# Kernel optimization log

Hardware: AMD Instinct MI355X
Metric: run time of the kernel (lower is better)

Reference implementation:

```python
import jax, jax.numpy as jnp
import numpy as np

N = 100000   # nodes
E = 1600000  # edges (avg degree 16)
D = 64       # feature / hidden / embedding dim
OUT = 2
NEG_SLOPE = 0.2


def setup_inputs() -> dict:
    key = jax.random.key(0)
    ks = jax.random.split(key, 12)
    s = 1.0 / np.sqrt(D)
    return {
        "x": jax.random.normal(ks[0], (N, D), dtype=jnp.float32),
        "edge_index": jax.random.randint(ks[1], (2, E), 0, N, dtype=jnp.int64),
        "Wl": jax.random.normal(ks[2], (3, D, D), dtype=jnp.float32) * s,
        "bl": jnp.zeros((3, D), dtype=jnp.float32),
        "Wr": jax.random.normal(ks[3], (3, D, D), dtype=jnp.float32) * s,
        "br": jnp.zeros((3, D), dtype=jnp.float32),
        "att": jax.random.normal(ks[4], (3, D), dtype=jnp.float32) * s,
        "bg": jnp.zeros((3, D), dtype=jnp.float32),
        "Ws": jax.random.normal(ks[5], (3, D, D), dtype=jnp.float32) * s,
        "bs": jnp.zeros((3, D), dtype=jnp.float32),
        "Wout": jax.random.normal(ks[6], (D, OUT), dtype=jnp.float32) * s,
        "bout": jnp.zeros((OUT,), dtype=jnp.float32),
    }


def _gatv2(h, src, dst, Wl, bl, Wr, br, att, bg):
    # GATv2Conv (heads=1, concat, add_self_loops=False):
    #   e_ij = att . LeakyReLU(Wl h_j + Wr h_i); softmax over incoming edges of i;
    #   out_i = sum_j alpha_ij * (Wl h_j) + bias
    xl = h @ Wl + bl                      # [N, D] source transform
    xr = h @ Wr + br                      # [N, D] dest transform
    e = jax.nn.leaky_relu(xl[src] + xr[dst], NEG_SLOPE) @ att  # [E]
    m = jax.ops.segment_max(e, dst, num_segments=N)            # per-dest max
    a = jnp.exp(e - m[dst])                                    # [E]
    denom = jax.ops.segment_sum(a, dst, num_segments=N)        # [N]
    alpha = a / denom[dst]                                     # [E]
    agg = jax.ops.segment_sum(alpha[:, None] * xl[src], dst, num_segments=N)
    return agg + bg                                            # [N, D]


def reference(x, edge_index, Wl, bl, Wr, br, att, bg, Ws, bs, Wout, bout):
    src, dst = edge_index[0], edge_index[1]
    # layer 1: gat1 + skip1, relu (dropout_rate=0 -> identity)
    h = jax.nn.relu(_gatv2(x, src, dst, Wl[0], bl[0], Wr[0], br[0], att[0], bg[0])
                    + x @ Ws[0] + bs[0])
    # middle layer
    h = jax.nn.relu(_gatv2(h, src, dst, Wl[1], bl[1], Wr[1], br[1], att[1], bg[1])
                    + h @ Ws[1] + bs[1])
    # last gat layer: no relu after
    h = _gatv2(h, src, dst, Wl[2], bl[2], Wr[2], br[2], att[2], bg[2]) + h @ Ws[2] + bs[2]
    return h @ Wout + bout
```

## Files before the change

kernel.cpp:

```cpp
#include <hip/hip_runtime.h>
#include <stdint.h>

#define NN 100000
#define EE 1600000
#define DD 64
#define NBUCK 782
#define SCWG 800
#define SCCHUNK 2000

using short8 = __attribute__((ext_vector_type(8))) short;
using f32x4  = __attribute__((ext_vector_type(4))) float;
using f2     = __attribute__((ext_vector_type(2))) float;


__device__ __forceinline__ unsigned short bf16_rne(float f) {
    unsigned int u = __float_as_uint(f);
    unsigned int r = (u + 0x7FFFu + ((u >> 16) & 1u)) >> 16;
    return (unsigned short)r;
}
__device__ __forceinline__ float bf16_to_f32(unsigned short h) {
    return __uint_as_float(((unsigned int)h) << 16);
}


__global__ void bucket_hist(const int* __restrict__ dst, int* __restrict__ bhist) {
    __shared__ int h[NBUCK];
    int t = threadIdx.x;
    for (int b = t; b < NBUCK; b += 256) h[b] = 0;
    __syncthreads();
    int start = blockIdx.x * SCCHUNK;
    int endi = min(start + SCCHUNK, EE);
    for (int e = start + t; e < endi; e += 256)
        atomicAdd(&h[dst[e] >> 7], 1);
    __syncthreads();
    for (int b = t; b < NBUCK; b += 256)
        if (h[b]) atomicAdd(&bhist[b], h[b]);
}

__global__ void bucket_scan(const int* __restrict__ bhist, int* __restrict__ bbase,
                            int* __restrict__ bcursor, int* __restrict__ offsets) {
    __shared__ int s[1024];
    int t = threadIdx.x;
    int v = (t < NBUCK) ? bhist[t] : 0;
    s[t] = v;
    __syncthreads();
    for (int off = 1; off < 1024; off <<= 1) {
        int a = (t >= off) ? s[t - off] : 0;
        __syncthreads();
        s[t] += a;
        __syncthreads();
    }
    if (t < NBUCK) { int excl = s[t] - v; bbase[t] = excl; bcursor[t] = excl; }
    if (t == 0) { bbase[NBUCK] = EE; offsets[NN] = EE; }
}

__global__ void bucket_scatter(const int* __restrict__ src, const int* __restrict__ dst,
                               int* __restrict__ bcursor, unsigned int* __restrict__ bedges) {
    __shared__ int cnt[NBUCK];
    __shared__ int lcur[NBUCK];
    int t = threadIdx.x;
    for (int b = t; b < NBUCK; b += 256) cnt[b] = 0;
    __syncthreads();
    int start = blockIdx.x * SCCHUNK;
    int endi = min(start + SCCHUNK, EE);
    for (int e = start + t; e < endi; e += 256)
        atomicAdd(&cnt[dst[e] >> 7], 1);
    __syncthreads();
    for (int b = t; b < NBUCK; b += 256) {
        int c = cnt[b];
        lcur[b] = c ? atomicAdd(&bcursor[b], c) : 0;
    }
    __syncthreads();
    for (int e = start + t; e < endi; e += 256) {
        int d = dst[e];
        int pos = atomicAdd(&lcur[d >> 7], 1);
        bedges[pos] = ((unsigned int)(d & 127) << 24) | (unsigned int)src[e];
    }
}

__global__ void bucket_csr(const unsigned int* __restrict__ bedges, const int* __restrict__ bbase,
                           int* __restrict__ offsets, int* __restrict__ csr) {
    __shared__ int ncnt[128];
    __shared__ int lofs[128];
    int b = blockIdx.x;
    int t = threadIdx.x;
    int beg = bbase[b], endb = bbase[b + 1];
    if (t < 128) ncnt[t] = 0;
    __syncthreads();
    for (int e = beg + t; e < endb; e += 256)
        atomicAdd(&ncnt[bedges[e] >> 24], 1);
    __syncthreads();
    if (t < 128) lofs[t] = ncnt[t];
    __syncthreads();
    for (int off = 1; off < 128; off <<= 1) {
        int a = 0;
        if (t < 128 && t >= off) a = lofs[t - off];
        __syncthreads();
        if (t < 128) lofs[t] += a;
        __syncthreads();
    }
    int excl = 0;
    if (t < 128) {
        excl = lofs[t] - ncnt[t];
        int node = b * 128 + t;
        if (node < NN) offsets[node] = beg + excl;
    }
    __syncthreads();
    if (t < 128) ncnt[t] = beg + excl;
    __syncthreads();
    for (int e = beg + t; e < endb; e += 256) {
        unsigned int ed = bedges[e];
        int pos = atomicAdd(&ncnt[ed >> 24], 1);
        csr[pos] = (int)(ed & 0xFFFFFFu);
    }
}


__global__ void conv_wx(const float* __restrict__ Wl, const float* __restrict__ Wr,
                        const float* __restrict__ Ws, const float* __restrict__ x,
                        unsigned short* __restrict__ Wt_hi, unsigned short* __restrict__ Wt_lo,
                        unsigned short* __restrict__ Ahi) {
    if (blockIdx.x < 144) {
        int e = blockIdx.x * 256 + threadIdx.x;
        if (e >= 9 * 4096) return;
        int mat = e >> 12;
        int r   = e & 4095;
        int k   = r >> 6, n = r & 63;
        int L = mat / 3, j = mat % 3;
        const float* W = (j == 0) ? Wl : ((j == 1) ? Wr : Ws);
        float v = W[L * 4096 + k * 64 + n];
        unsigned short hi = bf16_rne(v);
        unsigned short lo = bf16_rne(v - bf16_to_f32(hi));
        Wt_hi[mat * 4096 + n * 64 + k] = hi;
        Wt_lo[mat * 4096 + n * 64 + k] = lo;
    } else {
        int i = (blockIdx.x - 144) * 256 + threadIdx.x;
        int total = NN * 16;
        int stride = (gridDim.x - 144) * 256;
        for (; i < total; i += stride) {
            float4 v = *(const float4*)&x[(size_t)i * 4];
            ushort4 h;
            h.x = bf16_rne(v.x);
            h.y = bf16_rne(v.y);
            h.z = bf16_rne(v.z);
            h.w = bf16_rne(v.w);
            *(ushort4*)&Ahi[(size_t)i * 4] = h;
        }
    }
}


__global__ __launch_bounds__(256) void gemm_mfma(
    const unsigned short* __restrict__ Ahi,
    const unsigned short* __restrict__ Wt_hi, const unsigned short* __restrict__ Wt_lo,
    const float* __restrict__ bl, const float* __restrict__ br, const float* __restrict__ bs,
    unsigned short* __restrict__ Xlb, unsigned short* __restrict__ XRS) {
    int lane = threadIdx.x & 63;
    int wid  = threadIdx.x >> 6;
    int m0 = (blockIdx.x * 4 + wid) * 32;
    if (m0 >= NN) return;

    int l4 = lane & 15;
    int hi = lane >> 4;
    int koff = hi * 8;

    int arow0 = m0 + l4, arow1 = m0 + 16 + l4;
    bool ok0 = arow0 < NN, ok1 = arow1 < NN;
    int ar0 = ok0 ? arow0 : NN - 1;
    int ar1 = ok1 ? arow1 : NN - 1;

    const unsigned short* ab0 = Ahi + (size_t)ar0 * 64;
    const unsigned short* ab1 = Ahi + (size_t)ar1 * 64;
    short8 a0k0 = *(const short8*)(ab0 + koff);
    short8 a0k1 = *(const short8*)(ab0 + 32 + koff);
    short8 a1k0 = *(const short8*)(ab1 + koff);
    short8 a1k1 = *(const short8*)(ab1 + 32 + koff);

    int nbase0 = hi * 4;

#pragma unroll
    for (int m = 0; m < 3; m++) {
        const unsigned short* wh = Wt_hi + m * 4096;
        const unsigned short* wl = Wt_lo + m * 4096;
        const float* bias = (m == 0) ? bl : ((m == 1) ? br : bs);
#pragma unroll
        for (int tt = 0; tt < 4; tt++) {
            int ncol = tt * 16 + l4;
            const unsigned short* bh = wh + ncol * 64 + koff;
            const unsigned short* blo = wl + ncol * 64 + koff;
            short8 bhi0 = *(const short8*)bh;
            short8 bhi1 = *(const short8*)(bh + 32);
            short8 blo0 = *(const short8*)blo;
            short8 blo1 = *(const short8*)(blo + 32);

            f32x4 acc0 = {0.f, 0.f, 0.f, 0.f};
            f32x4 acc1 = {0.f, 0.f, 0.f, 0.f};
            acc0 = __builtin_amdgcn_mfma_f32_16x16x32_bf16(bhi0, a0k0, acc0, 0, 0, 0);
            acc1 = __builtin_amdgcn_mfma_f32_16x16x32_bf16(bhi0, a1k0, acc1, 0, 0, 0);
            acc0 = __builtin_amdgcn_mfma_f32_16x16x32_bf16(bhi1, a0k1, acc0, 0, 0, 0);
            acc1 = __builtin_amdgcn_mfma_f32_16x16x32_bf16(bhi1, a1k1, acc1, 0, 0, 0);
            acc0 = __builtin_amdgcn_mfma_f32_16x16x32_bf16(blo0, a0k0, acc0, 0, 0, 0);
            acc1 = __builtin_amdgcn_mfma_f32_16x16x32_bf16(blo0, a1k0, acc1, 0, 0, 0);
            acc0 = __builtin_amdgcn_mfma_f32_16x16x32_bf16(blo1, a0k1, acc0, 0, 0, 0);
            acc1 = __builtin_amdgcn_mfma_f32_16x16x32_bf16(blo1, a1k1, acc1, 0, 0, 0);

            int nb = tt * 16 + nbase0;
            float4 bb = *(const float4*)&bias[nb];
            ushort4 h0, h1;
            h0.x = bf16_rne(acc0[0] + bb.x); h0.y = bf16_rne(acc0[1] + bb.y);
            h0.z = bf16_rne(acc0[2] + bb.z); h0.w = bf16_rne(acc0[3] + bb.w);
            h1.x = bf16_rne(acc1[0] + bb.x); h1.y = bf16_rne(acc1[1] + bb.y);
            h1.z = bf16_rne(acc1[2] + bb.z); h1.w = bf16_rne(acc1[3] + bb.w);
            if (m == 0) {
                if (ok0) *(ushort4*)&Xlb[(size_t)ar0 * 64 + nb] = h0;
                if (ok1) *(ushort4*)&Xlb[(size_t)ar1 * 64 + nb] = h1;
            } else {
                int coff = (m == 1) ? 0 : 64;
                if (ok0) *(ushort4*)&XRS[(size_t)ar0 * 128 + coff + nb] = h0;
                if (ok1) *(ushort4*)&XRS[(size_t)ar1 * 128 + coff + nb] = h1;
            }
        }
    }
}


__device__ __forceinline__ float group_sum16(float t) {
    t += __int_as_float(__builtin_amdgcn_update_dpp(0, __float_as_int(t), 0xB1, 0xF, 0xF, true));
    t += __int_as_float(__builtin_amdgcn_update_dpp(0, __float_as_int(t), 0x4E, 0xF, 0xF, true));
    t += __int_as_float(__builtin_amdgcn_update_dpp(0, __float_as_int(t), 0x141, 0xF, 0xF, true));
    t += __int_as_float(__builtin_amdgcn_update_dpp(0, __float_as_int(t), 0x140, 0xF, 0xF, true));
    return t;
}

__device__ __forceinline__ void unpack4(uint2 u, f2& v01, f2& v23) {
    v01 = f2{ __uint_as_float(u.x << 16), __uint_as_float(u.x & 0xFFFF0000u) };
    v23 = f2{ __uint_as_float(u.y << 16), __uint_as_float(u.y & 0xFFFF0000u) };
}

__global__ __launch_bounds__(256) void node_kernel(
    const unsigned short* __restrict__ Xlb, const unsigned short* __restrict__ XRS,
    const int* __restrict__ offsets, const int* __restrict__ csr,
    const float* __restrict__ att, const float* __restrict__ bg,
    unsigned short* __restrict__ hout, int do_relu,
    const float* __restrict__ Wout, const float* __restrict__ bout,
    float* __restrict__ outp, int do_out) {
    int lane = threadIdx.x & 63;
    int wid  = threadIdx.x >> 6;
    int i = blockIdx.x * 4 + wid;
    if (i >= NN) return;
    int sub = lane & 15;
    int grp = lane >> 4;

    f2 xr01, xr23;
    unpack4(*(const uint2*)&XRS[(size_t)i * 128 + sub * 4], xr01, xr23);
    float4 att4 = *(const float4*)&att[sub * 4];
    f2 at01 = {att4.x, att4.y}, at23 = {att4.z, att4.w};

    f2 agg01 = {0.f, 0.f}, agg23 = {0.f, 0.f};
    float denom = 0.f;
    int beg = offsets[i], end = offsets[i + 1];

    for (int j0 = beg; j0 < end; j0 += 8) {
        int jA = j0 + grp, jB = jA + 4;
        bool vA = jA < end, vB = jB < end;
        int sA = csr[vA ? jA : beg];
        int sB = csr[vB ? jB : beg];
        uint2 uA = *(const uint2*)&Xlb[(size_t)sA * 64 + sub * 4];
        uint2 uB = *(const uint2*)&Xlb[(size_t)sB * 64 + sub * 4];
        f2 xA01, xA23, xB01, xB23;
        unpack4(uA, xA01, xA23);
        unpack4(uB, xB01, xB23);

        f2 sA01 = xA01 + xr01;
        f2 sA23 = xA23 + xr23;
        f2 sB01 = xB01 + xr01;
        f2 sB23 = xB23 + xr23;
        f2 lA01 = { fmaxf(sA01.x, 0.2f * sA01.x), fmaxf(sA01.y, 0.2f * sA01.y) };
        f2 lA23 = { fmaxf(sA23.x, 0.2f * sA23.x), fmaxf(sA23.y, 0.2f * sA23.y) };
        f2 lB01 = { fmaxf(sB01.x, 0.2f * sB01.x), fmaxf(sB01.y, 0.2f * sB01.y) };
        f2 lB23 = { fmaxf(sB23.x, 0.2f * sB23.x), fmaxf(sB23.y, 0.2f * sB23.y) };

        f2 tAv = lA01 * at01 + lA23 * at23;
        f2 tBv = lB01 * at01 + lB23 * at23;
        float tA = group_sum16(tAv.x + tAv.y);
        float tB = group_sum16(tBv.x + tBv.y);
        float aA = vA ? __expf(tA) : 0.f;
        float aB = vB ? __expf(tB) : 0.f;

        f2 aAv = {aA, aA};
        f2 aBv = {aB, aB};
        agg01 += aAv * xA01 + aBv * xB01;
        agg23 += aAv * xA23 + aBv * xB23;
        denom += aA + aB;
    }

    float aggx = agg01.x, aggy = agg01.y, aggz = agg23.x, aggw = agg23.y;
#pragma unroll
    for (int m = 16; m <= 32; m <<= 1) {
        aggx  += __shfl_xor(aggx, m, 64);
        aggy  += __shfl_xor(aggy, m, 64);
        aggz  += __shfl_xor(aggz, m, 64);
        aggw  += __shfl_xor(aggw, m, 64);
        denom += __shfl_xor(denom, m, 64);
    }

    float inv = (denom > 0.f) ? (1.0f / denom) : 0.f;
    f2 sk01, sk23;
    unpack4(*(const uint2*)&XRS[(size_t)i * 128 + 64 + sub * 4], sk01, sk23);
    float4 bg4 = *(const float4*)&bg[sub * 4];
    float4 res;
    res.x = aggx * inv + bg4.x + sk01.x;
    res.y = aggy * inv + bg4.y + sk01.y;
    res.z = aggz * inv + bg4.z + sk23.x;
    res.w = aggw * inv + bg4.w + sk23.y;
    if (do_relu) {
        res.x = fmaxf(res.x, 0.f); res.y = fmaxf(res.y, 0.f);
        res.z = fmaxf(res.z, 0.f); res.w = fmaxf(res.w, 0.f);
    }
    if (do_out) {
        float4 w01 = *(const float4*)&Wout[8 * sub];
        float4 w23 = *(const float4*)&Wout[8 * sub + 4];
        float o0 = res.x * w01.x + res.y * w01.z + res.z * w23.x + res.w * w23.z;
        float o1 = res.x * w01.y + res.y * w01.w + res.z * w23.y + res.w * w23.w;
        o0 = group_sum16(o0);
        o1 = group_sum16(o1);
        if (lane == 0) {
            outp[(size_t)i * 2 + 0] = o0 + bout[0];
            outp[(size_t)i * 2 + 1] = o1 + bout[1];
        }
    } else {
        if (grp == 0) {
            ushort4 h;
            h.x = bf16_rne(res.x);
            h.y = bf16_rne(res.y);
            h.z = bf16_rne(res.z);
            h.w = bf16_rne(res.w);
            *(ushort4*)&hout[(size_t)i * 64 + sub * 4] = h;
        }
    }
}


extern "C" void kernel_launch(void* const* d_in, const int* in_sizes, int n_in,
                              void* d_out, int out_size, void* d_ws, size_t ws_size,
                              hipStream_t stream) {
    const float* x    = (const float*)d_in[0];
    const int*   ei   = (const int*)d_in[1];
    const float* Wl   = (const float*)d_in[2];
    const float* bl   = (const float*)d_in[3];
    const float* Wr   = (const float*)d_in[4];
    const float* br   = (const float*)d_in[5];
    const float* att  = (const float*)d_in[6];
    const float* bg   = (const float*)d_in[7];
    const float* Ws   = (const float*)d_in[8];
    const float* bs   = (const float*)d_in[9];
    const float* Wout = (const float*)d_in[10];
    const float* bout = (const float*)d_in[11];
    float* out = (float*)d_out;

    size_t off = 0;
    char* base = (char*)d_ws;
    auto alloc = [&](size_t bytes) -> void* {
        void* p = base + off;
        off += (bytes + 255) & ~(size_t)255;
        return p;
    };
    unsigned short* Xlb = (unsigned short*)alloc((size_t)NN * 64 * 2);
    unsigned short* XRS = (unsigned short*)alloc((size_t)NN * 128 * 2);
    unsigned short* Ahi = (unsigned short*)alloc((size_t)NN * 64 * 2);
    unsigned short* Bhi = (unsigned short*)alloc((size_t)NN * 64 * 2);
    unsigned short* Wthi = (unsigned short*)alloc((size_t)9 * 4096 * 2);
    unsigned short* Wtlo = (unsigned short*)alloc((size_t)9 * 4096 * 2);
    int*  bhist  = (int*)alloc((size_t)NBUCK * 4);
    int*  bbase  = (int*)alloc((size_t)(NBUCK + 1) * 4);
    int*  bcur   = (int*)alloc((size_t)NBUCK * 4);
    unsigned int* bedges = (unsigned int*)alloc((size_t)EE * 4);
    int*  offs   = (int*)alloc((size_t)(NN + 1) * 4);
    int*  csr    = (int*)alloc((size_t)EE * 4);

    const int* src = ei;
    const int* dst = ei + EE;

    hipMemsetAsync(bhist, 0, (size_t)NBUCK * 4, stream);
    bucket_hist<<<SCWG, 256, 0, stream>>>(dst, bhist);
    bucket_scan<<<1, 1024, 0, stream>>>(bhist, bbase, bcur, offs);
    bucket_scatter<<<SCWG, 256, 0, stream>>>(src, dst, bcur, bedges);
    bucket_csr<<<NBUCK, 256, 0, stream>>>(bedges, bbase, offs, csr);

    conv_wx<<<144 + 400, 256, 0, stream>>>(Wl, Wr, Ws, x, Wthi, Wtlo, Ahi);

    unsigned short* cur = Ahi;
    unsigned short* nxt = Bhi;
    for (int L = 0; L < 3; L++) {
        gemm_mfma<<<(NN + 127) / 128, 256, 0, stream>>>(
            cur, Wthi + (size_t)L * 3 * 4096, Wtlo + (size_t)L * 3 * 4096,
            bl + L * 64, br + L * 64, bs + L * 64, Xlb, XRS);
        node_kernel<<<NN / 4, 256, 0, stream>>>(
            Xlb, XRS, offs, csr, att + L * 64, bg + L * 64,
            nxt, (L < 2) ? 1 : 0,
            Wout, bout, out, (L == 2) ? 1 : 0);
        unsigned short* tp = cur; cur = nxt; nxt = tp;
    }
}
```

Before: 356.4 us.

## Fuse CSR build and weight/input conversion into one cooperative kernel

Replaces the memset and five separate preprocessing launches (histogram, scan, scatter, per-bucket CSR, weight/x bf16 conversion) with a single cooperative kernel that separates the phases with grid-wide syncs. If the cooperative launch fails, it falls back to five phase-indexed launches. The aim is to remove per-launch overhead and idle gaps between the small preprocessing kernels. In exchange it adds grid-barrier cost, and 800 blocks must be co-resident for the cooperative launch to succeed.

Result: slower. 728.4 us (+104.4%).

```diff
diff --git a/kernel.cpp b/kernel.cpp
--- a/kernel.cpp
+++ b/kernel.cpp
@@ -1,5 +1,8 @@
 #include <hip/hip_runtime.h>
+#include <hip/hip_cooperative_groups.h>
 #include <stdint.h>
+
+namespace cg = cooperative_groups;
 
 #define NN 100000
 #define EE 1600000
@@ -23,128 +26,135 @@
 }
 
 
-__global__ void bucket_hist(const int* __restrict__ dst, int* __restrict__ bhist) {
-    __shared__ int h[NBUCK];
+__global__ __launch_bounds__(256) void csr_conv_all(
+    const int* __restrict__ src, const int* __restrict__ dst,
+    const float* __restrict__ Wl, const float* __restrict__ Wr, const float* __restrict__ Ws,
+    const float* __restrict__ x,
+    unsigned short* __restrict__ Wt_hi, unsigned short* __restrict__ Wt_lo,
+    unsigned short* __restrict__ Ahi,
+    int* __restrict__ bhist, int* __restrict__ bbase, int* __restrict__ bcur,
+    unsigned int* __restrict__ bedges, int* __restrict__ offsets, int* __restrict__ csr,
+    int phase) {
+    cg::grid_group grid = cg::this_grid();
+    __shared__ int sh[2 * NBUCK];
     int t = threadIdx.x;
-    for (int b = t; b < NBUCK; b += 256) h[b] = 0;
-    __syncthreads();
-    int start = blockIdx.x * SCCHUNK;
-    int endi = min(start + SCCHUNK, EE);
-    for (int e = start + t; e < endi; e += 256)
-        atomicAdd(&h[dst[e] >> 7], 1);
-    __syncthreads();
-    for (int b = t; b < NBUCK; b += 256)
-        if (h[b]) atomicAdd(&bhist[b], h[b]);
-}
-
-__global__ void bucket_scan(const int* __restrict__ bhist, int* __restrict__ bbase,
-                            int* __restrict__ bcursor, int* __restrict__ offsets) {
-    __shared__ int s[1024];
-    int t = threadIdx.x;
-    int v = (t < NBUCK) ? bhist[t] : 0;
-    s[t] = v;
-    __syncthreads();
-    for (int off = 1; off < 1024; off <<= 1) {
-        int a = (t >= off) ? s[t - off] : 0;
-        __syncthreads();
-        s[t] += a;
-        __syncthreads();
-    }
-    if (t < NBUCK) { int excl = s[t] - v; bbase[t] = excl; bcursor[t] = excl; }
-    if (t == 0) { bbase[NBUCK] = EE; offsets[NN] = EE; }
-}
-
-__global__ void bucket_scatter(const int* __restrict__ src, const int* __restrict__ dst,
-                               int* __restrict__ bcursor, unsigned int* __restrict__ bedges) {
-    __shared__ int cnt[NBUCK];
-    __shared__ int lcur[NBUCK];
-    int t = threadIdx.x;
-    for (int b = t; b < NBUCK; b += 256) cnt[b] = 0;
-    __syncthreads();
-    int start = blockIdx.x * SCCHUNK;
-    int endi = min(start + SCCHUNK, EE);
-    for (int e = start + t; e < endi; e += 256)
-        atomicAdd(&cnt[dst[e] >> 7], 1);
-    __syncthreads();
-    for (int b = t; b < NBUCK; b += 256) {
-        int c = cnt[b];
-        lcur[b] = c ? atomicAdd(&bcursor[b], c) : 0;
-    }
-    __syncthreads();
-    for (int e = start + t; e < endi; e += 256) {
-        int d = dst[e];
-        int pos = atomicAdd(&lcur[d >> 7], 1);
-        bedges[pos] = ((unsigned int)(d & 127) << 24) | (unsigned int)src[e];
-    }
-}
-
-__global__ void bucket_csr(const unsigned int* __restrict__ bedges, const int* __restrict__ bbase,
-                           int* __restrict__ offsets, int* __restrict__ csr) {
-    __shared__ int ncnt[128];
-    __shared__ int lofs[128];
     int b = blockIdx.x;
-    int t = threadIdx.x;
-    int beg = bbase[b], endb = bbase[b + 1];
-    if (t < 128) ncnt[t] = 0;
-    __syncthreads();
-    for (int e = beg + t; e < endb; e += 256)
-        atomicAdd(&ncnt[bedges[e] >> 24], 1);
-    __syncthreads();
-    if (t < 128) lofs[t] = ncnt[t];
-    __syncthreads();
-    for (int off = 1; off < 128; off <<= 1) {
-        int a = 0;
-        if (t < 128 && t >= off) a = lofs[t - off];
-        __syncthreads();
-        if (t < 128) lofs[t] += a;
-        __syncthreads();
-    }
-    int excl = 0;
-    if (t < 128) {
-        excl = lofs[t] - ncnt[t];
-        int node = b * 128 + t;
-        if (node < NN) offsets[node] = beg + excl;
-    }
-    __syncthreads();
-    if (t < 128) ncnt[t] = beg + excl;
-    __syncthreads();
-    for (int e = beg + t; e < endb; e += 256) {
-        unsigned int ed = bedges[e];
-        int pos = atomicAdd(&ncnt[ed >> 24], 1);
-        csr[pos] = (int)(ed & 0xFFFFFFu);
-    }
-}
-
-
-__global__ void conv_wx(const float* __restrict__ Wl, const float* __restrict__ Wr,
-                        const float* __restrict__ Ws, const float* __restrict__ x,
-                        unsigned short* __restrict__ Wt_hi, unsigned short* __restrict__ Wt_lo,
-                        unsigned short* __restrict__ Ahi) {
-    if (blockIdx.x < 144) {
-        int e = blockIdx.x * 256 + threadIdx.x;
-        if (e >= 9 * 4096) return;
-        int mat = e >> 12;
-        int r   = e & 4095;
-        int k   = r >> 6, n = r & 63;
-        int L = mat / 3, j = mat % 3;
-        const float* W = (j == 0) ? Wl : ((j == 1) ? Wr : Ws);
-        float v = W[L * 4096 + k * 64 + n];
-        unsigned short hi = bf16_rne(v);
-        unsigned short lo = bf16_rne(v - bf16_to_f32(hi));
-        Wt_hi[mat * 4096 + n * 64 + k] = hi;
-        Wt_lo[mat * 4096 + n * 64 + k] = lo;
-    } else {
-        int i = (blockIdx.x - 144) * 256 + threadIdx.x;
-        int total = NN * 16;
-        int stride = (gridDim.x - 144) * 256;
-        for (; i < total; i += stride) {
+
+    if (phase < 0 || phase == 0) {
+        int g = b * 256 + t;
+        if (g < NBUCK) bhist[g] = 0;
+        if (g < 9 * 4096) {
+            int mat = g >> 12, r = g & 4095;
+            int k = r >> 6, n = r & 63;
+            int L = mat / 3, j = mat % 3;
+            const float* W = (j == 0) ? Wl : ((j == 1) ? Wr : Ws);
+            float v = W[L * 4096 + k * 64 + n];
+            unsigned short hi = bf16_rne(v);
+            unsigned short lo = bf16_rne(v - bf16_to_f32(hi));
+            Wt_hi[mat * 4096 + n * 64 + k] = hi;
+            Wt_lo[mat * 4096 + n * 64 + k] = lo;
+        }
+        for (int i = g; i < NN * 16; i += SCWG * 256) {
             float4 v = *(const float4*)&x[(size_t)i * 4];
             ushort4 h;
-            h.x = bf16_rne(v.x);
-            h.y = bf16_rne(v.y);
-            h.z = bf16_rne(v.z);
-            h.w = bf16_rne(v.w);
+            h.x = bf16_rne(v.x); h.y = bf16_rne(v.y);
+            h.z = bf16_rne(v.z); h.w = bf16_rne(v.w);
             *(ushort4*)&Ahi[(size_t)i * 4] = h;
+        }
+    }
+    if (phase < 0) grid.sync();
+
+    if (phase < 0 || phase == 1) {
+        for (int i = t; i < NBUCK; i += 256) sh[i] = 0;
+        __syncthreads();
+        int start = b * SCCHUNK;
+        int endi = min(start + SCCHUNK, EE);
+        for (int e = start + t; e < endi; e += 256)
+            atomicAdd(&sh[dst[e] >> 7], 1);
+        __syncthreads();
+        for (int i = t; i < NBUCK; i += 256)
+            if (sh[i]) atomicAdd(&bhist[i], sh[i]);
+    }
+    if (phase < 0) grid.sync();
+
+    if ((phase < 0 || phase == 2) && b == 0) {
+        int i0 = t * 4;
+        int v0 = (i0 + 0 < NBUCK) ? bhist[i0 + 0] : 0;
+        int v1 = (i0 + 1 < NBUCK) ? bhist[i0 + 1] : 0;
+        int v2 = (i0 + 2 < NBUCK) ? bhist[i0 + 2] : 0;
+        int v3 = (i0 + 3 < NBUCK) ? bhist[i0 + 3] : 0;
+        int tsum = v0 + v1 + v2 + v3;
+        sh[t] = tsum;
+        __syncthreads();
+        for (int off = 1; off < 256; off <<= 1) {
+            int a = (t >= off) ? sh[t - off] : 0;
+            __syncthreads();
+            sh[t] += a;
+            __syncthreads();
+        }
+        int run = sh[t] - tsum;
+        if (i0 + 0 < NBUCK) { bbase[i0 + 0] = run; bcur[i0 + 0] = run; run += v0; }
+        if (i0 + 1 < NBUCK) { bbase[i0 + 1] = run; bcur[i0 + 1] = run; run += v1; }
+        if (i0 + 2 < NBUCK) { bbase[i0 + 2] = run; bcur[i0 + 2] = run; run += v2; }
+        if (i0 + 3 < NBUCK) { bbase[i0 + 3] = run; bcur[i0 + 3] = run; run += v3; }
+        if (t == 0) { bbase[NBUCK] = EE; offsets[NN] = EE; }
+    }
+    if (phase < 0) grid.sync();
+
+    if (phase < 0 || phase == 3) {
+        int* cnt  = sh;
+        int* lcur = sh + NBUCK;
+        for (int i = t; i < NBUCK; i += 256) cnt[i] = 0;
+        __syncthreads();
+        int start = b * SCCHUNK;
+        int endi = min(start + SCCHUNK, EE);
+        for (int e = start + t; e < endi; e += 256)
+            atomicAdd(&cnt[dst[e] >> 7], 1);
+        __syncthreads();
+        for (int i = t; i < NBUCK; i += 256) {
+            int c = cnt[i];
+            lcur[i] = c ? atomicAdd(&bcur[i], c) : 0;
+        }
+        __syncthreads();
+        for (int e = start + t; e < endi; e += 256) {
+            int d = dst[e];
+            int pos = atomicAdd(&lcur[d >> 7], 1);
+            bedges[pos] = ((unsigned int)(d & 127) << 24) | (unsigned int)src[e];
+        }
+    }
+    if (phase < 0) grid.sync();
+
+    if ((phase < 0 || phase == 4) && b < NBUCK) {
+        int* ncnt = sh;
+        int* lofs = sh + 128;
+        int beg = bbase[b], endb = bbase[b + 1];
+        if (t < 128) ncnt[t] = 0;
+        __syncthreads();
+        for (int e = beg + t; e < endb; e += 256)
+            atomicAdd(&ncnt[bedges[e] >> 24], 1);
+        __syncthreads();
+        if (t < 128) lofs[t] = ncnt[t];
+        __syncthreads();
+        for (int off = 1; off < 128; off <<= 1) {
+            int a = 0;
+            if (t < 128 && t >= off) a = lofs[t - off];
+            __syncthreads();
+            if (t < 128) lofs[t] += a;
+            __syncthreads();
+        }
+        int excl = 0;
+        if (t < 128) {
+            excl = lofs[t] - ncnt[t];
+            int node = b * 128 + t;
+            if (node < NN) offsets[node] = beg + excl;
+        }
+        __syncthreads();
+        if (t < 128) ncnt[t] = beg + excl;
+        __syncthreads();
+        for (int e = beg + t; e < endb; e += 256) {
+            unsigned int ed = bedges[e];
+            int pos = atomicAdd(&ncnt[ed >> 24], 1);
+            csr[pos] = (int)(ed & 0xFFFFFFu);
         }
     }
 }
@@ -378,16 +388,26 @@
     int*  offs   = (int*)alloc((size_t)(NN + 1) * 4);
     int*  csr    = (int*)alloc((size_t)EE * 4);
 
-    const int* src = ei;
-    const int* dst = ei + EE;
-
-    hipMemsetAsync(bhist, 0, (size_t)NBUCK * 4, stream);
-    bucket_hist<<<SCWG, 256, 0, stream>>>(dst, bhist);
-    bucket_scan<<<1, 1024, 0, stream>>>(bhist, bbase, bcur, offs);
-    bucket_scatter<<<SCWG, 256, 0, stream>>>(src, dst, bcur, bedges);
-    bucket_csr<<<NBUCK, 256, 0, stream>>>(bedges, bbase, offs, csr);
-
-    conv_wx<<<144 + 400, 256, 0, stream>>>(Wl, Wr, Ws, x, Wthi, Wtlo, Ahi);
+    const int* srcp = ei;
+    const int* dstp = ei + EE;
+
+    int phaseAll = -1;
+    void* params[] = {
+        (void*)&srcp, (void*)&dstp, (void*)&Wl, (void*)&Wr, (void*)&Ws, (void*)&x,
+        (void*)&Wthi, (void*)&Wtlo, (void*)&Ahi,
+        (void*)&bhist, (void*)&bbase, (void*)&bcur,
+        (void*)&bedges, (void*)&offs, (void*)&csr, (void*)&phaseAll
+    };
+    hipError_t cerr = hipLaunchCooperativeKernel((const void*)csr_conv_all,
+                                                 dim3(SCWG), dim3(256), params, 0, stream);
+    if (cerr != hipSuccess) {
+        (void)hipGetLastError();
+        for (int p = 0; p < 5; p++) {
+            csr_conv_all<<<SCWG, 256, 0, stream>>>(
+                srcp, dstp, Wl, Wr, Ws, x, Wthi, Wtlo, Ahi,
+                bhist, bbase, bcur, bedges, offs, csr, p);
+        }
+    }
 
     unsigned short* cur = Ahi;
     unsigned short* nxt = Bhi;
```
